# Kernel optimization log

Measured on AMD Instinct MI355X. Metric: run time of the kernel, lower is better.

The kernel has to match this reference:

```python
import jax, jax.numpy as jnp
import numpy as np

B, T, R = 256, 20, 100          # batch, decode steps, image regions
IN_DIM, NUM_HID, V_DIM = 300, 1024, 2048
VOCAB = 10000


def _p(key, shape, scale=0.02):
    return (jax.random.normal(key, shape, dtype=jnp.float32) * scale)


def setup_inputs() -> dict:
    key = jax.random.key(0)
    ks = jax.random.split(key, 24)
    H4 = 4 * NUM_HID
    return {
        "caption": jax.random.randint(ks[0], (B, T - 1), 0, VOCAB),
        "features": jax.random.normal(ks[1], (B, R, V_DIM), dtype=jnp.float32),
        # word embedding table
        "emb": _p(ks[2], (VOCAB, IN_DIM)),
        # v_input: Linear(v_dim, in_dim)
        "W_vin": _p(ks[3], (V_DIM, IN_DIM)), "b_vin": jnp.zeros((IN_DIM,), jnp.float32),
        # rnn_v: LSTMCell(in_dim + num_hid + v_dim, num_hid); weights stored [in, 4H]
        "W_ih_v": _p(ks[4], (IN_DIM + NUM_HID + V_DIM, H4)),
        "W_hh_v": _p(ks[5], (NUM_HID, H4)),
        "b_v": jnp.zeros((H4,), jnp.float32),
        # attention MLP
        "W_va": _p(ks[6], (V_DIM, NUM_HID)), "b_va": jnp.zeros((NUM_HID,), jnp.float32),
        "W_ha": _p(ks[7], (NUM_HID, NUM_HID)), "b_ha": jnp.zeros((NUM_HID,), jnp.float32),
        "W_a": _p(ks[8], (NUM_HID, 1)), "b_a": jnp.zeros((1,), jnp.float32),
        # rnn_c: LSTMCell(num_hid + v_dim, num_hid)
        "W_ih_c": _p(ks[9], (NUM_HID + V_DIM, H4)),
        "W_hh_c": _p(ks[10], (NUM_HID, H4)),
        "b_c": jnp.zeros((H4,), jnp.float32),
        # classifier: Linear(num_hid, vocab)
        "W_cls": _p(ks[11], (NUM_HID, VOCAB)), "b_cls": jnp.zeros((VOCAB,), jnp.float32),
    }


def _lstm_cell(x, h, c, W_ih, W_hh, b):
    # torch LSTMCell gate order: i, f, g, o
    g = x @ W_ih + h @ W_hh + b
    i, f, gg, o = jnp.split(g, 4, axis=-1)
    c2 = jax.nn.sigmoid(f) * c + jax.nn.sigmoid(i) * jnp.tanh(gg)
    h2 = jax.nn.sigmoid(o) * jnp.tanh(c2)
    return h2, c2


def reference(caption, features, emb, W_vin, b_vin, W_ih_v, W_hh_v, b_v,
              W_va, b_va, W_ha, b_ha, W_a, b_a, W_ih_c, W_hh_c, b_c,
              W_cls, b_cls):
    cap_emb = emb[caption]                                  # [B, T-1, in_dim]
    feat_mean = jnp.mean(features, axis=1)                  # [B, v_dim]
    v_rnn_inp = feat_mean @ W_vin + b_vin                   # [B, in_dim]
    x = jnp.concatenate([v_rnn_inp[:, None, :], cap_emb], axis=1)  # [B, T, in_dim]
    # precompute region projection (loop-invariant in the original)
    va = features @ W_va + b_va                             # [B, R, num_hid]

    def step(carry, x_t):
        h_v, c_v, h_c, c_c = carry
        inp_v = jnp.concatenate([feat_mean, h_c, x_t], axis=1)
        h_v, c_v = _lstm_cell(inp_v, h_v, c_v, W_ih_v, W_hh_v, b_v)
        ha = h_v @ W_ha + b_ha                              # [B, num_hid]
        att_logit = jnp.tanh(va + ha[:, None, :]) @ W_a + b_a  # [B, R, 1]
        att = jax.nn.softmax(att_logit, axis=1)             # softmax over regions
        feat_hat = jnp.mean(features * att, axis=1)         # [B, v_dim] (mean, as in torch)
        inp_c = jnp.concatenate([feat_hat, h_v], axis=1)
        h_c, c_c = _lstm_cell(inp_c, h_c, c_c, W_ih_c, W_hh_c, b_c)
        return (h_v, c_v, h_c, c_c), (h_c, att)

    z = jnp.zeros((x.shape[0], NUM_HID), jnp.float32)
    _, (outs, atts) = jax.lax.scan(step, (z, z, z, z), jnp.swapaxes(x, 0, 1))
    outputs = jnp.swapaxes(outs, 0, 1)                      # [B, T, num_hid]
    attention = jnp.swapaxes(atts, 0, 1)                    # [B, T, R, 1]
    repr_ = outputs @ W_cls + b_cls                         # [B, T, vocab]
    return repr_, attention
```

## Files before the change

kernel.cpp:

```cpp
#include <hip/hip_runtime.h>
#include <math.h>

namespace {

constexpr int NB  = 256;
constexpr int NT  = 20;
constexpr int NR  = 100;
constexpr int IND = 300;
constexpr int NH  = 1024;
constexpr int VD  = 2048;
constexpr int H4  = 4096;
constexpr int VOC = 10000;
constexpr int VOCP = 10112;

constexpr int KGV = 2368;
constexpr int KGC = 4096;
constexpr int KHA = 1024;
constexpr int KCL = 1024;
constexpr int KFM = 2048;
constexpr int NVI = 384;
constexpr int A2VLD = 2048;
constexpr int X2LD  = 320;

constexpr int ZGV = 4;  constexpr int KSV = 608;
constexpr int ZGC = 4;  constexpr int KSC = 1024;
constexpr int ZHA = 8;  constexpr int KSH = 128;
constexpr int ZFM = 8;  constexpr int KSF = 256;

typedef short  s8v  __attribute__((ext_vector_type(8)));
typedef float  f4v  __attribute__((ext_vector_type(4)));

__device__ __forceinline__ float sigm(float x) { return 1.f / (1.f + expf(-x)); }
__device__ __forceinline__ unsigned short f2b(float x) {
  return __builtin_bit_cast(unsigned short, (__bf16)x);
}
__device__ __forceinline__ float b2f(unsigned short u) {
  return (float)__builtin_bit_cast(__bf16, u);
}
__device__ __forceinline__ int Frow(int row) { return (row ^ (row >> 2)) & 3; }
__device__ __forceinline__ void store1(unsigned short* rowbase, int k, float x, int Fs) {
  rowbase[k ^ Fs] = f2b(x);
}

__device__ __forceinline__ void gload16(const unsigned short* g, unsigned short* l) {
  __builtin_amdgcn_global_load_lds(
      (const __attribute__((address_space(1))) void*)g,
      (__attribute__((address_space(3))) void*)l, 16, 0, 0);
}

#define BARRIER()  __syncthreads()
#define VMWAIT0()  asm volatile("s_waitcnt vmcnt(0)" ::: "memory")

template<bool OUT_BF16>
__global__ __launch_bounds__(256)
void gemm128(const unsigned short* __restrict__ A, int lda,
             const unsigned short* __restrict__ Bt, int ldb,
             void* __restrict__ Cv, int ldc,
             const float* __restrict__ bias,
             int N, int Kp)
{
  __shared__ unsigned short As[2][128 * 32];
  __shared__ unsigned short Bs[2][128 * 32];
  const int tid = threadIdx.x, wid = tid >> 6, lane = tid & 63;
  const int wm = (wid >> 1) * 64, wn = (wid & 1) * 64;
  const int m0 = blockIdx.x * 128, n0 = blockIdx.y * 128;
  const int sr = tid >> 2, sc = (tid & 3) * 8;
  const unsigned short* a0 = A + (size_t)(m0 + sr) * lda + sc;
  const unsigned short* a1 = a0 + (size_t)64 * lda;
  const unsigned short* b0 = Bt + (size_t)(n0 + sr) * ldb + sc;
  const unsigned short* b1 = b0 + (size_t)64 * ldb;
  const int rr = lane & 15;
  const int kc = (((lane >> 4) ^ Frow(rr)) & 3) * 8;

  f4v acc[4][4] = {};

  auto stage = [&](int s, int k) {
    gload16(a0 + k, &As[s][tid * 8]);
    gload16(a1 + k, &As[s][2048 + tid * 8]);
    gload16(b0 + k, &Bs[s][tid * 8]);
    gload16(b1 + k, &Bs[s][2048 + tid * 8]);
  };
  auto compute = [&](int s) {
    s8v a[4], b[4];
#pragma unroll
    for (int i = 0; i < 4; ++i) a[i] = *(const s8v*)&As[s][(wm + i * 16 + rr) * 32 + kc];
#pragma unroll
    for (int j = 0; j < 4; ++j) b[j] = *(const s8v*)&Bs[s][(wn + j * 16 + rr) * 32 + kc];
#pragma unroll
    for (int i = 0; i < 4; ++i)
#pragma unroll
      for (int j = 0; j < 4; ++j)
        acc[i][j] = __builtin_amdgcn_mfma_f32_16x16x32_bf16(a[i], b[j], acc[i][j], 0, 0, 0);
  };

  stage(0, 0);
  VMWAIT0();
  BARRIER();

  int cur = 0;
  for (int k0 = 0; k0 < Kp; k0 += 32) {
    if (k0 + 32 < Kp) stage(cur ^ 1, k0 + 32);
    compute(cur);
    VMWAIT0();
    BARRIER();
    cur ^= 1;
  }

  const int cr = (lane >> 4) * 4, cc = lane & 15;
#pragma unroll
  for (int i = 0; i < 4; ++i) {
#pragma unroll
    for (int j = 0; j < 4; ++j) {
      const int gn = n0 + wn + j * 16 + cc;
      if (gn >= N) continue;
#pragma unroll
      for (int r = 0; r < 4; ++r) {
        const int gm = m0 + wm + i * 16 + cr + r;
        float v = acc[i][j][r] + bias[gn];
        if constexpr (OUT_BF16) ((unsigned short*)Cv)[(size_t)gm * ldc + gn] = f2b(v);
        else                    ((float*)Cv)[(size_t)gm * ldc + gn] = v;
      }
    }
  }
}

template<bool XSEG, int BN>
__global__ __launch_bounds__(256)
void gemm_sk2(const unsigned short* __restrict__ A, int lda,
              const unsigned short* __restrict__ X2, int t,
              const unsigned short* __restrict__ Bt, int ldb,
              float* __restrict__ P, int N, int Kp, int Ksplit)
{
  constexpr int FN = BN / 32;
  __shared__ unsigned short As[2][128 * 32];
  __shared__ unsigned short Bs[2][BN * 32];
  const int tid = threadIdx.x, wid = tid >> 6, lane = tid & 63;
  const int wm = (wid >> 1) * 64, wn = (wid & 1) * (BN / 2);
  const int m0 = blockIdx.y * 128, n0 = blockIdx.x * BN;
  const int kbeg = blockIdx.z * Ksplit;
  const int kend = min(Kp, kbeg + Ksplit);
  const int sr = tid >> 2, sc = (tid & 3) * 8;
  const unsigned short* a0 = A + (size_t)(m0 + sr) * lda + sc;
  const unsigned short* a1 = a0 + (size_t)64 * lda;
  const unsigned short* x0 = nullptr;
  const unsigned short* x1 = nullptr;
  if constexpr (XSEG) {
    x0 = X2 + ((size_t)(m0 + sr) * NT + t) * X2LD + sc;
    x1 = x0 + (size_t)64 * NT * X2LD;
  }
  const unsigned short* b0 = Bt + (size_t)(n0 + sr) * ldb + sc;
  const unsigned short* b1 = b0 + (size_t)64 * ldb;
  const int rr = lane & 15;
  const int kc = (((lane >> 4) ^ Frow(rr)) & 3) * 8;

  f4v acc[4][FN] = {};

  auto stage = [&](int s, int k) {
    if constexpr (XSEG) {
      if (k >= A2VLD) {
        gload16(x0 + (k - A2VLD), &As[s][tid * 8]);
        gload16(x1 + (k - A2VLD), &As[s][2048 + tid * 8]);
      } else {
        gload16(a0 + k, &As[s][tid * 8]);
        gload16(a1 + k, &As[s][2048 + tid * 8]);
      }
    } else {
      gload16(a0 + k, &As[s][tid * 8]);
      gload16(a1 + k, &As[s][2048 + tid * 8]);
    }
    gload16(b0 + k, &Bs[s][tid * 8]);
    if constexpr (BN == 128) gload16(b1 + k, &Bs[s][2048 + tid * 8]);
  };
  auto compute = [&](int s) {
    s8v a[4], b[FN];
#pragma unroll
    for (int i = 0; i < 4; ++i) a[i] = *(const s8v*)&As[s][(wm + i * 16 + rr) * 32 + kc];
#pragma unroll
    for (int j = 0; j < FN; ++j) b[j] = *(const s8v*)&Bs[s][(wn + j * 16 + rr) * 32 + kc];
#pragma unroll
    for (int i = 0; i < 4; ++i)
#pragma unroll
      for (int j = 0; j < FN; ++j)
        acc[i][j] = __builtin_amdgcn_mfma_f32_16x16x32_bf16(a[i], b[j], acc[i][j], 0, 0, 0);
  };

  stage(0, kbeg);
  VMWAIT0();
  BARRIER();

  int cur = 0;
  for (int k0 = kbeg; k0 < kend; k0 += 32) {
    if (k0 + 32 < kend) stage(cur ^ 1, k0 + 32);
    compute(cur);
    VMWAIT0();
    BARRIER();
    cur ^= 1;
  }

  float* out = P + (size_t)blockIdx.z * 256 * N;
  const int cr = (lane >> 4) * 4, cc = lane & 15;
#pragma unroll
  for (int i = 0; i < 4; ++i)
#pragma unroll
    for (int j = 0; j < FN; ++j)
#pragma unroll
      for (int r = 0; r < 4; ++r)
        out[(size_t)(m0 + wm + i * 16 + cr + r) * N + n0 + wn + j * 16 + cc] = acc[i][j][r];
}

__global__ __launch_bounds__(256)
void gemm_va_f32(const float* __restrict__ A, int lda,
                 const unsigned short* __restrict__ Bt, int ldb,
                 unsigned short* __restrict__ C, int ldc,
                 const float* __restrict__ bias, int N, int Kp)
{
  __shared__ unsigned short As[128 * 32];
  __shared__ unsigned short Bs[128 * 32];
  const int tid = threadIdx.x, wid = tid >> 6, lane = tid & 63;
  const int wm = (wid >> 1) * 64, wn = (wid & 1) * 64;
  const int m0 = blockIdx.x * 128, n0 = blockIdx.y * 128;
  const unsigned short* bsrc0 = Bt + (size_t)(n0 + (tid >> 2)) * ldb + (tid & 3) * 8;
  const unsigned short* bsrc1 = bsrc0 + (size_t)64 * ldb;
  const int rr = lane & 15;
  const int kc = (((lane >> 4) ^ Frow(rr)) & 3) * 8;

  f4v acc[4][4] = {};
  for (int k0 = 0; k0 < Kp; k0 += 32) {
#pragma unroll
    for (int it = 0; it < 4; ++it) {
      const int r = it * 32 + (tid >> 3), c = (tid & 7) * 4;
      const float4 v = *(const float4*)(A + (size_t)(m0 + r) * lda + k0 + c);
      ushort4 w;
      w.x = f2b(v.x); w.y = f2b(v.y); w.z = f2b(v.z); w.w = f2b(v.w);
      *(ushort4*)&As[r * 32 + (c ^ (Frow(r & 15) << 3))] = w;
    }
    gload16(bsrc0 + k0, &Bs[tid * 8]);
    gload16(bsrc1 + k0, &Bs[2048 + tid * 8]);
    __syncthreads();
    s8v a[4], b[4];
#pragma unroll
    for (int i = 0; i < 4; ++i) a[i] = *(const s8v*)&As[(wm + i * 16 + rr) * 32 + kc];
#pragma unroll
    for (int j = 0; j < 4; ++j) b[j] = *(const s8v*)&Bs[(wn + j * 16 + rr) * 32 + kc];
#pragma unroll
    for (int i = 0; i < 4; ++i)
#pragma unroll
      for (int j = 0; j < 4; ++j)
        acc[i][j] = __builtin_amdgcn_mfma_f32_16x16x32_bf16(a[i], b[j], acc[i][j], 0, 0, 0);
    __syncthreads();
  }
  const int cr = (lane >> 4) * 4, cc = lane & 15;
#pragma unroll
  for (int i = 0; i < 4; ++i)
#pragma unroll
    for (int j = 0; j < 4; ++j) {
      const int gn = n0 + wn + j * 16 + cc;
      if (gn >= N) continue;
#pragma unroll
      for (int r = 0; r < 4; ++r)
        C[(size_t)(m0 + wm + i * 16 + cr + r) * ldc + gn] = f2b(acc[i][j][r] + bias[gn]);
    }
}

__global__ void convB_k(const float* __restrict__ src, int srcld, int K, int N,
                        unsigned short* __restrict__ dst, int dstld, int coff)
{
  __shared__ float t[32][33];
  const int kb = blockIdx.x * 32, nb = blockIdx.y * 32;
  const int tx = threadIdx.x & 31, ty = threadIdx.x >> 5;
#pragma unroll
  for (int i = 0; i < 32; i += 8) {
    const int k = kb + ty + i, n = nb + tx;
    t[ty + i][tx] = (k < K && n < N) ? src[(size_t)k * srcld + n] : 0.f;
  }
  __syncthreads();
#pragma unroll
  for (int i = 0; i < 32; i += 8) {
    const int n = nb + ty + i, k = kb + tx;
    if (n >= N || k >= K) continue;
    unsigned short* row = dst + (size_t)n * dstld;
    row[(coff + k) ^ (Frow(n & 15) << 3)] = f2b(t[tx][ty + i]);
  }
}

__global__ void zpad_swz_k(unsigned short* __restrict__ dst, int ld, int c0, int N)
{
  const int w = ld - c0;
  const int idx = blockIdx.x * 256 + threadIdx.x;
  if (idx >= N * w) return;
  const int n = idx / w, c = c0 + (idx % w);
  dst[(size_t)n * ld + (c ^ (Frow(n & 15) << 3))] = 0;
}

__global__ void zfill_k(unsigned short* __restrict__ p, int n)
{
  const int i = blockIdx.x * 256 + threadIdx.x;
  if (i < n) p[i] = 0;
}

__global__ void feat_pass_k(const float* __restrict__ feat,
                            unsigned short* __restrict__ fm16,
                            unsigned short* __restrict__ f16out)
{
  const int idx = blockIdx.x * 256 + threadIdx.x;
  if (idx >= NB * (VD / 8)) return;
  const int d0 = (idx & (VD / 8 - 1)) * 8, b = idx / (VD / 8);
  const float* base = feat + (size_t)b * NR * VD + d0;
  float s[8] = {};
  for (int r = 0; r < NR; ++r) {
    const float4 x0 = *(const float4*)(base + (size_t)r * VD);
    const float4 x1 = *(const float4*)(base + (size_t)r * VD + 4);
    s[0] += x0.x; s[1] += x0.y; s[2] += x0.z; s[3] += x0.w;
    s[4] += x1.x; s[5] += x1.y; s[6] += x1.z; s[7] += x1.w;
    if (f16out) {
      unsigned short w[8] = {f2b(x0.x), f2b(x0.y), f2b(x0.z), f2b(x0.w),
                             f2b(x1.x), f2b(x1.y), f2b(x1.z), f2b(x1.w)};
      const int ro = b * NR + r;
      *(s8v*)(f16out + (size_t)ro * VD + (d0 ^ (Frow(ro & 15) << 3))) = *(const s8v*)w;
    }
  }
  unsigned short w[8];
#pragma unroll
  for (int e = 0; e < 8; ++e) w[e] = f2b(s[e] * (1.f / NR));
  *(s8v*)(fm16 + (size_t)b * KFM + (d0 ^ (Frow(b & 15) << 3))) = *(const s8v*)w;
}

__global__ void fmg_red_k(const float* __restrict__ gp, const float* __restrict__ bv,
                          float* __restrict__ fmg)
{
  const int idx = blockIdx.x * 256 + threadIdx.x;
  if (idx >= NB * H4) return;
  float s = bv[idx & (H4 - 1)];
#pragma unroll
  for (int z = 0; z < ZFM; ++z) s += gp[(size_t)z * NB * H4 + idx];
  fmg[idx] = s;
}

__global__ void vinp_red_k(const float* __restrict__ gp, const float* __restrict__ bvin,
                           float* __restrict__ vinp)
{
  const int idx = blockIdx.x * 256 + threadIdx.x;
  if (idx >= NB * IND) return;
  const int n = idx % IND, b = idx / IND;
  float s = bvin[n];
#pragma unroll
  for (int z = 0; z < ZFM; ++z) s += gp[(size_t)z * NB * NVI + (size_t)b * NVI + n];
  vinp[idx] = s;
}

__global__ void build_x2_k(const int* __restrict__ cap, const float* __restrict__ emb,
                           const float* __restrict__ vinp, unsigned short* __restrict__ X2)
{
  const int idx = blockIdx.x * 256 + threadIdx.x;
  if (idx >= NB * NT * X2LD) return;
  const int c = idx % X2LD;
  const int bt = idx / X2LD;
  const int t = bt % NT, b = bt / NT;
  const int Fs = Frow(b & 15) << 3;
  unsigned short val = 0;
  if (c < IND) {
    const float v = (t == 0) ? vinp[b * IND + c]
                             : emb[(size_t)cap[b * (NT - 1) + (t - 1)] * IND + c];
    val = f2b(v);
  }
  X2[(size_t)bt * X2LD + (c ^ Fs)] = val;
}

__global__ void lstm_pw_v_k(const float* __restrict__ gp, const float* __restrict__ fmg,
                            float* __restrict__ cv,
                            unsigned short* __restrict__ A2c, unsigned short* __restrict__ A2v)
{
  const int idx = blockIdx.x * 256 + threadIdx.x;
  if (idx >= NB * NH) return;
  const int n = idx & (NH - 1), b = idx >> 10;
  const size_t base = (size_t)b * H4;
  float gi = fmg[base + n], gf = fmg[base + NH + n];
  float gg = fmg[base + 2 * NH + n], go = fmg[base + 3 * NH + n];
#pragma unroll
  for (int z = 0; z < ZGV; ++z) {
    const float* g = gp + (size_t)z * NB * H4 + base;
    gi += g[n]; gf += g[NH + n]; gg += g[2 * NH + n]; go += g[3 * NH + n];
  }
  const float c2 = sigm(gf) * cv[idx] + sigm(gi) * tanhf(gg);
  const float h2 = sigm(go) * tanhf(c2);
  cv[idx] = c2;
  const int Fs = Frow(b & 15) << 3;
  store1(A2c + (size_t)b * KGC, 2048 + n, h2, Fs);
  store1(A2v + (size_t)b * A2VLD, 1024 + n, h2, Fs);
}

__global__ void lstm_pw_c_k(const float* __restrict__ gp, const float* __restrict__ bc,
                            float* __restrict__ cc,
                            unsigned short* __restrict__ A2v, unsigned short* __restrict__ A2c,
                            unsigned short* __restrict__ outh2, int t)
{
  const int idx = blockIdx.x * 256 + threadIdx.x;
  if (idx >= NB * NH) return;
  const int n = idx & (NH - 1), b = idx >> 10;
  const size_t base = (size_t)b * H4;
  float gi = bc[n], gf = bc[NH + n], gg = bc[2 * NH + n], go = bc[3 * NH + n];
#pragma unroll
  for (int z = 0; z < ZGC; ++z) {
    const float* g = gp + (size_t)z * NB * H4 + base;
    gi += g[n]; gf += g[NH + n]; gg += g[2 * NH + n]; go += g[3 * NH + n];
  }
  const float c2 = sigm(gf) * cc[idx] + sigm(gi) * tanhf(gg);
  const float h2 = sigm(go) * tanhf(c2);
  cc[idx] = c2;
  const int Fs = Frow(b & 15) << 3;
  store1(A2v + (size_t)b * A2VLD, n, h2, Fs);
  store1(A2c + (size_t)b * KGC, 3072 + n, h2, Fs);
  const int ro = b * NT + t;
  store1(outh2 + (size_t)ro * KCL, n, h2, Frow(ro & 15) << 3);
}

template<bool F16>
__global__ __launch_bounds__(512)
void att_fused_k(const unsigned short* __restrict__ va16,
                 const float* __restrict__ hap,
                 const float* __restrict__ bha,
                 const float* __restrict__ Wa, const float* __restrict__ ba,
                 const unsigned short* __restrict__ f16,
                 const float* __restrict__ f32,
                 unsigned short* __restrict__ A2c,
                 float* __restrict__ att_out, int t)
{
  const int b = blockIdx.x, tid = threadIdx.x;
  const int lane = tid & 63, wid = tid >> 6;
  __shared__ float ha_s[NH];
  __shared__ float wa_s[NH];
  __shared__ float red_s[128];
  __shared__ float fh_s[2][VD];

  for (int j = tid; j < NH; j += 512) {
    float s = bha[j];
#pragma unroll
    for (int z = 0; z < ZHA; ++z) s += hap[((size_t)z * NB + b) * NH + j];
    ha_s[j] = s;
    wa_s[j] = Wa[j];
  }
  __syncthreads();

  for (int r = wid; r < NR; r += 8) {
    const unsigned short* vrow = va16 + ((size_t)b * NR + r) * NH + lane * 16;
    float s = 0.f;
#pragma unroll
    for (int u = 0; u < 2; ++u) {
      const s8v v = *(const s8v*)(vrow + u * 8);
      const int j0 = lane * 16 + u * 8;
#pragma unroll
      for (int e = 0; e < 8; ++e)
        s += tanhf(b2f((unsigned short)v[e]) + ha_s[j0 + e]) * wa_s[j0 + e];
    }
    for (int o = 32; o; o >>= 1) s += __shfl_down(s, o);
    if (lane == 0) red_s[r] = s + ba[0];
  }
  __syncthreads();

  if (wid == 0) {
    float v0 = (lane < NR) ? red_s[lane] : -3.4e38f;
    float v1 = (lane + 64 < NR) ? red_s[lane + 64] : -3.4e38f;
    float m = fmaxf(v0, v1);
    for (int o = 32; o; o >>= 1) m = fmaxf(m, __shfl_xor(m, o));
    const float e0 = (lane < NR) ? expf(v0 - m) : 0.f;
    const float e1 = (lane + 64 < NR) ? expf(v1 - m) : 0.f;
    float s = e0 + e1;
    for (int o = 32; o; o >>= 1) s += __shfl_xor(s, o);
    const float inv = 1.f / s;
    if (lane < NR) red_s[lane] = e0 * inv;
    if (lane + 64 < NR) red_s[lane + 64] = e1 * inv;
  }
  __syncthreads();
  if (tid < NR) att_out[((size_t)b * NT + t) * NR + tid] = red_s[tid];

  const int half = tid >> 8;
  const int dd = (tid & 255) * 8;
  const int r0 = half * 50, r1 = r0 + 50;
  float fh8[8] = {};
  if constexpr (F16) {
    const unsigned short* fbase = f16 + (size_t)b * NR * VD;
    for (int r = r0; r < r1; ++r) {
      const int ro = b * NR + r;
      const s8v f = *(const s8v*)(fbase + (size_t)r * VD + (dd ^ (Frow(ro & 15) << 3)));
      const float a = red_s[r];
#pragma unroll
      for (int e = 0; e < 8; ++e) fh8[e] += a * b2f((unsigned short)f[e]);
    }
  } else {
    const float* fb = f32 + (size_t)b * NR * VD + dd;
    for (int r = r0; r < r1; ++r) {
      const float4 x0 = *(const float4*)(fb + (size_t)r * VD);
      const float4 x1 = *(const float4*)(fb + (size_t)r * VD + 4);
      const float a = red_s[r];
      fh8[0] += a * x0.x; fh8[1] += a * x0.y; fh8[2] += a * x0.z; fh8[3] += a * x0.w;
      fh8[4] += a * x1.x; fh8[5] += a * x1.y; fh8[6] += a * x1.z; fh8[7] += a * x1.w;
    }
  }
#pragma unroll
  for (int e = 0; e < 8; ++e) fh_s[half][dd + e] = fh8[e];
  __syncthreads();

  unsigned short* rowbase = A2c + (size_t)b * KGC;
  const int Fs = Frow(b & 15) << 3;
  const int d0 = tid * 4;
#pragma unroll
  for (int e = 0; e < 4; ++e) {
    const float v = (fh_s[0][d0 + e] + fh_s[1][d0 + e]) * (1.f / NR);
    store1(rowbase, d0 + e, v, Fs);
  }
}

inline void convB(hipStream_t st, const float* src, int srcld, int K, int N,
                  unsigned short* dst, int dstld, int coff)
{
  dim3 g((K + 31) / 32, (N + 31) / 32);
  convB_k<<<g, 256, 0, st>>>(src, srcld, K, N, dst, dstld, coff);
}

}

extern "C" void kernel_launch(void* const* d_in, const int* in_sizes, int n_in,
                              void* d_out, int out_size, void* d_ws, size_t ws_size,
                              hipStream_t stream)
{
  const int*   caption = (const int*)  d_in[0];
  const float* feat    = (const float*)d_in[1];
  const float* emb     = (const float*)d_in[2];
  const float* W_vin   = (const float*)d_in[3];
  const float* b_vin   = (const float*)d_in[4];
  const float* W_ih_v  = (const float*)d_in[5];
  const float* W_hh_v  = (const float*)d_in[6];
  const float* b_v     = (const float*)d_in[7];
  const float* W_va    = (const float*)d_in[8];
  const float* b_va    = (const float*)d_in[9];
  const float* W_ha    = (const float*)d_in[10];
  const float* b_ha    = (const float*)d_in[11];
  const float* W_a     = (const float*)d_in[12];
  const float* b_a     = (const float*)d_in[13];
  const float* W_ih_c  = (const float*)d_in[14];
  const float* W_hh_c  = (const float*)d_in[15];
  const float* b_c     = (const float*)d_in[16];
  const float* W_cls   = (const float*)d_in[17];
  const float* b_cls   = (const float*)d_in[18];

  float* out_repr = (float*)d_out;
  float* out_att  = out_repr + (size_t)NB * NT * VOC;

  char* cur = (char*)d_ws;
  auto take = [&](size_t bytes) { char* p = cur; cur += bytes; return p; };

  unsigned short* A2v  = (unsigned short*)take((size_t)NB * A2VLD * 2);
  unsigned short* A2c  = (unsigned short*)take((size_t)NB * KGC * 2);
  float* CV            = (float*)take((size_t)NB * NH * 4);
  float* CC            = (float*)take((size_t)NB * NH * 4);
  const size_t ZERO_BYTES = (size_t)NB * A2VLD * 2 + (size_t)NB * KGC * 2
                          + 2 * (size_t)NB * NH * 4;

  float* VINP          = (float*)take((size_t)NB * IND * 4);
  unsigned short* X2   = (unsigned short*)take((size_t)NB * NT * X2LD * 2);
  float* FMG           = (float*)take((size_t)NB * H4 * 4);
  unsigned short* FM16 = (unsigned short*)take((size_t)NB * KFM * 2);
  unsigned short* VA16 = (unsigned short*)take((size_t)NB * NR * NH * 2);
  float* GP            = (float*)take((size_t)8 * NB * H4 * 4);
  float* HAP           = (float*)take((size_t)ZHA * NB * NH * 4);
  unsigned short* OUTH2= (unsigned short*)take((size_t)NB * NT * KCL * 2);
  unsigned short* Wgv2t= (unsigned short*)take((size_t)H4 * KGV * 2);
  unsigned short* Wha2t= (unsigned short*)take((size_t)NH * KHA * 2);
  unsigned short* Wgc2t= (unsigned short*)take((size_t)H4 * KGC * 2);
  unsigned short* Wfmg = (unsigned short*)take((size_t)H4 * KFM * 2);
  unsigned short* WvinT= (unsigned short*)take((size_t)NVI * KFM * 2);
  unsigned short* Wcls2t=(unsigned short*)take((size_t)VOCP * KCL * 2);
  unsigned short* Wva16t=(unsigned short*)take((size_t)NH * VD * 2);
  unsigned short* FEAT16=(unsigned short*)cur;
  const bool useF16 = ((size_t)(cur - (char*)d_ws) + (size_t)NB * NR * VD * 2) <= ws_size;

  hipMemsetAsync(A2v, 0, ZERO_BYTES, stream);

  convB(stream, W_ih_v + (size_t)2048 * H4, H4, 1024, H4, Wgv2t, KGV, 0);
  convB(stream, W_hh_v,                     H4, 1024, H4, Wgv2t, KGV, 1024);
  convB(stream, W_ih_v + (size_t)3072 * H4, H4, 300,  H4, Wgv2t, KGV, 2048);
  zpad_swz_k<<<((H4 * (KGV - 2348)) + 255) / 256, 256, 0, stream>>>(
      Wgv2t, KGV, 2348, H4);
  convB(stream, W_ha, NH, 1024, NH, Wha2t, KHA, 0);
  convB(stream, W_ih_c,                     H4, 2048, H4, Wgc2t, KGC, 0);
  convB(stream, W_ih_c + (size_t)2048 * H4, H4, 1024, H4, Wgc2t, KGC, 2048);
  convB(stream, W_hh_c,                     H4, 1024, H4, Wgc2t, KGC, 3072);
  convB(stream, W_ih_v,                     H4, 2048, H4, Wfmg,  KFM, 0);
  convB(stream, W_vin, IND, 2048, IND, WvinT, KFM, 0);
  zfill_k<<<(((NVI - IND) * KFM) + 255) / 256, 256, 0, stream>>>(
      WvinT + (size_t)IND * KFM, (NVI - IND) * KFM);
  convB(stream, W_cls, VOC, 1024, VOC, Wcls2t, KCL, 0);
  zfill_k<<<(((VOCP - VOC) * KCL) + 255) / 256, 256, 0, stream>>>(
      Wcls2t + (size_t)VOC * KCL, (VOCP - VOC) * KCL);
  convB(stream, W_va, NH, VD, NH, Wva16t, VD, 0);

  feat_pass_k<<<(NB * (VD / 8) + 255) / 256, 256, 0, stream>>>(
      feat, FM16, useF16 ? FEAT16 : nullptr);
  gemm_sk2<false, 128><<<dim3(NVI / 128, 2, ZFM), 256, 0, stream>>>(
      FM16, KFM, nullptr, 0, WvinT, KFM, GP, NVI, KFM, KSF);
  vinp_red_k<<<(NB * IND + 255) / 256, 256, 0, stream>>>(GP, b_vin, VINP);
  build_x2_k<<<(NB * NT * X2LD + 255) / 256, 256, 0, stream>>>(caption, emb, VINP, X2);
  gemm_sk2<false, 128><<<dim3(H4 / 128, 2, ZFM), 256, 0, stream>>>(
      FM16, KFM, nullptr, 0, Wfmg, KFM, GP, H4, KFM, KSF);
  fmg_red_k<<<(NB * H4 + 255) / 256, 256, 0, stream>>>(GP, b_v, FMG);
  if (useF16) {
    dim3 g((NB * NR) / 128, NH / 128);
    gemm128<true><<<g, 256, 0, stream>>>(
        FEAT16, VD, Wva16t, VD, VA16, NH, b_va, NH, VD);
  } else {
    dim3 g((NB * NR) / 128, NH / 128);
    gemm_va_f32<<<g, 256, 0, stream>>>(feat, VD, Wva16t, VD, VA16, NH, b_va, NH, VD);
  }

  for (int t = 0; t < NT; ++t) {
    gemm_sk2<true, 64><<<dim3(H4 / 64, 2, ZGV), 256, 0, stream>>>(
        A2v, A2VLD, X2, t, Wgv2t, KGV, GP, H4, KGV, KSV);
    lstm_pw_v_k<<<(NB * NH + 255) / 256, 256, 0, stream>>>(GP, FMG, CV, A2c, A2v);
    gemm_sk2<false, 64><<<dim3(NH / 64, 2, ZHA), 256, 0, stream>>>(
        A2c + 2048, KGC, nullptr, 0, Wha2t, KHA, HAP, NH, KHA, KSH);
    if (useF16)
      att_fused_k<true><<<NB, 512, 0, stream>>>(
          VA16, HAP, b_ha, W_a, b_a, FEAT16, nullptr, A2c, out_att, t);
    else
      att_fused_k<false><<<NB, 512, 0, stream>>>(
          VA16, HAP, b_ha, W_a, b_a, nullptr, feat, A2c, out_att, t);
    gemm_sk2<false, 64><<<dim3(H4 / 64, 2, ZGC), 256, 0, stream>>>(
        A2c, KGC, nullptr, 0, Wgc2t, KGC, GP, H4, KGC, KSC);
    lstm_pw_c_k<<<(NB * NH + 255) / 256, 256, 0, stream>>>(GP, b_c, CC, A2v, A2c, OUTH2, t);
  }

  {
    dim3 g((NB * NT) / 128, VOCP / 128);
    gemm128<false><<<g, 256, 0, stream>>>(
        OUTH2, KCL, Wcls2t, KCL, out_repr, VOC, b_cls, VOC, KCL);
  }
}
```

Measured before the change: 2.746 ms.

## Use full-batch M tile in per-step LSTM GEMMs and double split-K depth

The split-K GEMM gains a BM template parameter. The two per-step LSTM gate GEMMs now use a 256-row M tile covering the whole batch, so each weight tile is loaded from memory once instead of twice. To keep enough blocks in flight, the split-K factor doubles from 4 to 8. The MFMA inner loop also loads A fragments one at a time to limit register pressure. The cost is a larger accumulator per thread (8x2 fragments) and more partial sums for the following reduction to read.

```diff
diff --git a/kernel.cpp b/kernel.cpp
--- a/kernel.cpp
+++ b/kernel.cpp
@@ -22,8 +22,8 @@
 constexpr int A2VLD = 2048;
 constexpr int X2LD  = 320;
 
-constexpr int ZGV = 4;  constexpr int KSV = 608;
-constexpr int ZGC = 4;  constexpr int KSC = 1024;
+constexpr int ZGV = 8;  constexpr int KSV = 320;
+constexpr int ZGC = 8;  constexpr int KSC = 512;
 constexpr int ZHA = 8;  constexpr int KSH = 128;
 constexpr int ZFM = 8;  constexpr int KSF = 256;
 
@@ -81,16 +81,16 @@
     gload16(b1 + k, &Bs[s][2048 + tid * 8]);
   };
   auto compute = [&](int s) {
-    s8v a[4], b[4];
-#pragma unroll
-    for (int i = 0; i < 4; ++i) a[i] = *(const s8v*)&As[s][(wm + i * 16 + rr) * 32 + kc];
+    s8v b[4];
 #pragma unroll
     for (int j = 0; j < 4; ++j) b[j] = *(const s8v*)&Bs[s][(wn + j * 16 + rr) * 32 + kc];
 #pragma unroll
-    for (int i = 0; i < 4; ++i)
+    for (int i = 0; i < 4; ++i) {
+      const s8v av = *(const s8v*)&As[s][(wm + i * 16 + rr) * 32 + kc];
 #pragma unroll
       for (int j = 0; j < 4; ++j)
-        acc[i][j] = __builtin_amdgcn_mfma_f32_16x16x32_bf16(a[i], b[j], acc[i][j], 0, 0, 0);
+        acc[i][j] = __builtin_amdgcn_mfma_f32_16x16x32_bf16(av, b[j], acc[i][j], 0, 0, 0);
+    }
   };
 
   stage(0, 0);
@@ -124,64 +124,70 @@
   }
 }
 
-template<bool XSEG, int BN>
+template<bool XSEG, int BM, int BN>
 __global__ __launch_bounds__(256)
 void gemm_sk2(const unsigned short* __restrict__ A, int lda,
               const unsigned short* __restrict__ X2, int t,
               const unsigned short* __restrict__ Bt, int ldb,
               float* __restrict__ P, int N, int Kp, int Ksplit)
 {
+  constexpr int FM = BM / 32;
   constexpr int FN = BN / 32;
-  __shared__ unsigned short As[2][128 * 32];
+  constexpr int AG = BM / 64;
+  __shared__ unsigned short As[2][BM * 32];
   __shared__ unsigned short Bs[2][BN * 32];
   const int tid = threadIdx.x, wid = tid >> 6, lane = tid & 63;
-  const int wm = (wid >> 1) * 64, wn = (wid & 1) * (BN / 2);
-  const int m0 = blockIdx.y * 128, n0 = blockIdx.x * BN;
+  const int wm = (wid >> 1) * (BM / 2), wn = (wid & 1) * (BN / 2);
+  const int m0 = blockIdx.y * BM, n0 = blockIdx.x * BN;
   const int kbeg = blockIdx.z * Ksplit;
   const int kend = min(Kp, kbeg + Ksplit);
   const int sr = tid >> 2, sc = (tid & 3) * 8;
-  const unsigned short* a0 = A + (size_t)(m0 + sr) * lda + sc;
-  const unsigned short* a1 = a0 + (size_t)64 * lda;
-  const unsigned short* x0 = nullptr;
-  const unsigned short* x1 = nullptr;
-  if constexpr (XSEG) {
-    x0 = X2 + ((size_t)(m0 + sr) * NT + t) * X2LD + sc;
-    x1 = x0 + (size_t)64 * NT * X2LD;
+
+  const unsigned short* ap[AG];
+  const unsigned short* xp[AG];
+#pragma unroll
+  for (int g = 0; g < AG; ++g) {
+    ap[g] = A + (size_t)(m0 + sr + 64 * g) * lda + sc;
+    if constexpr (XSEG)
+      xp[g] = X2 + ((size_t)(m0 + sr + 64 * g) * NT + t) * X2LD + sc;
   }
   const unsigned short* b0 = Bt + (size_t)(n0 + sr) * ldb + sc;
   const unsigned short* b1 = b0 + (size_t)64 * ldb;
   const int rr = lane & 15;
   const int kc = (((lane >> 4) ^ Frow(rr)) & 3) * 8;
 
-  f4v acc[4][FN] = {};
+  f4v acc[FM][FN] = {};
 
   auto stage = [&](int s, int k) {
     if constexpr (XSEG) {
       if (k >= A2VLD) {
-        gload16(x0 + (k - A2VLD), &As[s][tid * 8]);
-        gload16(x1 + (k - A2VLD), &As[s][2048 + tid * 8]);
+#pragma unroll
+        for (int g = 0; g < AG; ++g)
+          gload16(xp[g] + (k - A2VLD), &As[s][g * 2048 + tid * 8]);
       } else {
-        gload16(a0 + k, &As[s][tid * 8]);
-        gload16(a1 + k, &As[s][2048 + tid * 8]);
+#pragma unroll
+        for (int g = 0; g < AG; ++g)
+          gload16(ap[g] + k, &As[s][g * 2048 + tid * 8]);
       }
     } else {
-      gload16(a0 + k, &As[s][tid * 8]);
-      gload16(a1 + k, &As[s][2048 + tid * 8]);
+#pragma unroll
+      for (int g = 0; g < AG; ++g)
+        gload16(ap[g] + k, &As[s][g * 2048 + tid * 8]);
     }
     gload16(b0 + k, &Bs[s][tid * 8]);
     if constexpr (BN == 128) gload16(b1 + k, &Bs[s][2048 + tid * 8]);
   };
   auto compute = [&](int s) {
-    s8v a[4], b[FN];
-#pragma unroll
-    for (int i = 0; i < 4; ++i) a[i] = *(const s8v*)&As[s][(wm + i * 16 + rr) * 32 + kc];
+    s8v b[FN];
 #pragma unroll
     for (int j = 0; j < FN; ++j) b[j] = *(const s8v*)&Bs[s][(wn + j * 16 + rr) * 32 + kc];
 #pragma unroll
-    for (int i = 0; i < 4; ++i)
+    for (int i = 0; i < FM; ++i) {
+      const s8v av = *(const s8v*)&As[s][(wm + i * 16 + rr) * 32 + kc];
 #pragma unroll
       for (int j = 0; j < FN; ++j)
-        acc[i][j] = __builtin_amdgcn_mfma_f32_16x16x32_bf16(a[i], b[j], acc[i][j], 0, 0, 0);
+        acc[i][j] = __builtin_amdgcn_mfma_f32_16x16x32_bf16(av, b[j], acc[i][j], 0, 0, 0);
+    }
   };
 
   stage(0, kbeg);
@@ -200,7 +206,7 @@
   float* out = P + (size_t)blockIdx.z * 256 * N;
   const int cr = (lane >> 4) * 4, cc = lane & 15;
 #pragma unroll
-  for (int i = 0; i < 4; ++i)
+  for (int i = 0; i < FM; ++i)
 #pragma unroll
     for (int j = 0; j < FN; ++j)
 #pragma unroll
@@ -596,11 +602,11 @@
 
   feat_pass_k<<<(NB * (VD / 8) + 255) / 256, 256, 0, stream>>>(
       feat, FM16, useF16 ? FEAT16 : nullptr);
-  gemm_sk2<false, 128><<<dim3(NVI / 128, 2, ZFM), 256, 0, stream>>>(
+  gemm_sk2<false, 128, 128><<<dim3(NVI / 128, 2, ZFM), 256, 0, stream>>>(
       FM16, KFM, nullptr, 0, WvinT, KFM, GP, NVI, KFM, KSF);
   vinp_red_k<<<(NB * IND + 255) / 256, 256, 0, stream>>>(GP, b_vin, VINP);
   build_x2_k<<<(NB * NT * X2LD + 255) / 256, 256, 0, stream>>>(caption, emb, VINP, X2);
-  gemm_sk2<false, 128><<<dim3(H4 / 128, 2, ZFM), 256, 0, stream>>>(
+  gemm_sk2<false, 128, 128><<<dim3(H4 / 128, 2, ZFM), 256, 0, stream>>>(
       FM16, KFM, nullptr, 0, Wfmg, KFM, GP, H4, KFM, KSF);
   fmg_red_k<<<(NB * H4 + 255) / 256, 256, 0, stream>>>(GP, b_v, FMG);
   if (useF16) {
@@ -613,10 +619,10 @@
   }
 
   for (int t = 0; t < NT; ++t) {
-    gemm_sk2<true, 64><<<dim3(H4 / 64, 2, ZGV), 256, 0, stream>>>(
+    gemm_sk2<true, 256, 64><<<dim3(H4 / 64, 1, ZGV), 256, 0, stream>>>(
         A2v, A2VLD, X2, t, Wgv2t, KGV, GP, H4, KGV, KSV);
     lstm_pw_v_k<<<(NB * NH + 255) / 256, 256, 0, stream>>>(GP, FMG, CV, A2c, A2v);
-    gemm_sk2<false, 64><<<dim3(NH / 64, 2, ZHA), 256, 0, stream>>>(
+    gemm_sk2<false, 128, 64><<<dim3(NH / 64, 2, ZHA), 256, 0, stream>>>(
         A2c + 2048, KGC, nullptr, 0, Wha2t, KHA, HAP, NH, KHA, KSH);
     if (useF16)
       att_fused_k<true><<<NB, 512, 0, stream>>>(
@@ -624,7 +630,7 @@
     else
       att_fused_k<false><<<NB, 512, 0, stream>>>(
           VA16, HAP, b_ha, W_a, b_a, nullptr, feat, A2c, out_att, t);
-    gemm_sk2<false, 64><<<dim3(H4 / 64, 2, ZGC), 256, 0, stream>>>(
+    gemm_sk2<false, 256, 64><<<dim3(H4 / 64, 1, ZGC), 256, 0, stream>>>(
         A2c, KGC, nullptr, 0, Wgc2t, KGC, GP, H4, KGC, KSC);
     lstm_pw_c_k<<<(NB * NH + 255) / 256, 256, 0, stream>>>(GP, b_c, CC, A2v, A2c, OUTH2, t);
   }
```

After: 2.760 ms. Within noise of the previous version (+0.5%).
